# Optimization experiments

Measured on AMD Instinct MI355X. Metric: run time of the kernel, lower is better.

## Reference

```python
import jax, jax.numpy as jnp
import numpy as np

HEADS, OUT_CH = 8, 32  # GATConv(128, 256//8, heads=8) -> concat width 256
NEG_SLOPE = 0.2


def setup_inputs() -> dict:
    key = jax.random.key(0)
    ks = jax.random.split(key, 12)
    N, E, F_IN = 50000, 500000, 128
    H, C = HEADS, OUT_CH
    HID = H * C            # 256
    x = jax.random.normal(ks[0], (N, F_IN), dtype=jnp.float32)
    edge_index = jax.random.randint(ks[1], (2, E), 0, N, dtype=jnp.int64)
    s = 1.0 / np.sqrt(F_IN)
    W_gat = jax.random.normal(ks[2], (F_IN, H * C), dtype=jnp.float32) * s
    att_src = jax.random.normal(ks[3], (H, C), dtype=jnp.float32) * (1.0 / np.sqrt(C))
    att_dst = jax.random.normal(ks[4], (H, C), dtype=jnp.float32) * (1.0 / np.sqrt(C))
    b_gat = jnp.zeros((HID,), dtype=jnp.float32)
    W1 = jax.random.normal(ks[5], (HID, HID // 2), dtype=jnp.float32) * (1.0 / np.sqrt(HID))
    b1 = jnp.zeros((HID // 2,), dtype=jnp.float32)
    W2 = jax.random.normal(ks[6], (HID // 2, 6), dtype=jnp.float32) * (1.0 / np.sqrt(HID // 2))
    b2 = jnp.zeros((6,), dtype=jnp.float32)
    return {"x": x, "edge_index": edge_index, "W_gat": W_gat, "att_src": att_src,
            "att_dst": att_dst, "b_gat": b_gat, "W1": W1, "b1": b1, "W2": W2, "b2": b2}


def _gat_forward(x, edge_index, W_gat, att_src, att_dst, b_gat):
    N = x.shape[0]
    H, C = HEADS, OUT_CH
    # add self loops (PyG GATConv default)
    loop = jnp.arange(N, dtype=edge_index.dtype)
    src = jnp.concatenate([edge_index[0], loop])
    dst = jnp.concatenate([edge_index[1], loop])
    # per-node transform: [N, H, C]
    xh = (x @ W_gat).reshape(N, H, C)
    a_src = jnp.einsum('nhc,hc->nh', xh, att_src)  # [N, H]
    a_dst = jnp.einsum('nhc,hc->nh', xh, att_dst)  # [N, H]
    alpha = a_src[src] + a_dst[dst]                # [Etot, H]
    alpha = jnp.where(alpha >= 0, alpha, NEG_SLOPE * alpha)  # leaky relu
    # segment softmax over destination nodes
    m = jax.ops.segment_max(alpha, dst, num_segments=N)     # [N, H]
    m = jax.lax.stop_gradient(m)
    ex = jnp.exp(alpha - m[dst])
    denom = jax.ops.segment_sum(ex, dst, num_segments=N)    # [N, H]
    coef = ex / denom[dst]                                   # [Etot, H]
    # weighted scatter-add aggregation
    msgs = xh[src] * coef[:, :, None]                        # [Etot, H, C]
    out = jax.ops.segment_sum(msgs, dst, num_segments=N)     # [N, H, C]
    return out.reshape(N, H * C) + b_gat


def reference(x, edge_index, W_gat, att_src, att_dst, b_gat, W1, b1, W2, b2):
    h = _gat_forward(x, edge_index, W_gat, att_src, att_dst, b_gat)
    h = jax.nn.elu(h)
    g = jnp.mean(h, axis=0, keepdims=True)   # [1, 256] mean pool
    g = jax.nn.relu(g @ W1 + b1)
    return g @ W2 + b2                        # [1, 6] logits
```

## Files before the change

### kernel.cpp

```cpp
#include <hip/hip_runtime.h>
#include <hip/hip_fp8.h>
#include <math.h>

#define F_IN 128
#define HID 256
#define NH 8
#define CAP 40
#define BCAP 4096

typedef _Float16 h16;
typedef __attribute__((ext_vector_type(8))) _Float16 half8;
typedef __attribute__((ext_vector_type(4))) float f32x4;

__device__ inline unsigned char f32_to_fp8(float v) {
#if __has_builtin(__builtin_amdgcn_cvt_pk_fp8_f32)
    return (unsigned char)(__builtin_amdgcn_cvt_pk_fp8_f32(v, v, 0, false) & 0xff);
#else
    __hip_fp8_e4m3 t(v);
    return (unsigned char)t.__x;
#endif
}

__device__ inline void fp8x4_to_f32(int w, float* out) {
#if __has_builtin(__builtin_amdgcn_cvt_pk_f32_fp8)
    auto lo = __builtin_amdgcn_cvt_pk_f32_fp8(w, false);
    auto hi = __builtin_amdgcn_cvt_pk_f32_fp8(w, true);
    out[0] = lo[0]; out[1] = lo[1]; out[2] = hi[0]; out[3] = hi[1];
#else
    #pragma unroll
    for (int k = 0; k < 4; ++k) {
        __hip_fp8_e4m3 t;
        t.__x = (unsigned char)((w >> (8 * k)) & 0xff);
        out[k] = (float)t;
    }
#endif
}

__global__ void k_prep(const float* __restrict__ Wg, h16* __restrict__ Wt_sw,
                       int* gcur, float* g2, int n) {
    int i = blockIdx.x * 256 + threadIdx.x;
    if (i < 256) gcur[i] = 0;
    if (i < 256 * HID) g2[i] = 0.f;
    if (i < 4096) {
        int fid = i;
        int lane16 = fid & 15;
        int quad = (fid >> 4) & 3;
        int ks = (fid >> 6) & 3;
        int ct = fid >> 8;
        int col = ct * 16 + lane16;
        int k0 = ks * 32 + quad * 8;
        half8 v;
        #pragma unroll
        for (int j = 0; j < 8; ++j) v[j] = (h16)Wg[(size_t)(k0 + j) * HID + col];
        *(half8*)(Wt_sw + (size_t)fid * 8) = v;
    }
}

__global__ __launch_bounds__(512) void k_ga(const float* __restrict__ x,
                                            const h16* __restrict__ Wt_sw,
                                            const float* __restrict__ att_s,
                                            const float* __restrict__ att_d,
                                            const int* __restrict__ dstp,
                                            const int* __restrict__ srcp,
                                            unsigned char* __restrict__ xh8,
                                            float* __restrict__ a_src,
                                            float* __restrict__ a_dst,
                                            unsigned int* __restrict__ gbuck,
                                            int* __restrict__ gcur,
                                            int n, int e, int ntiles,
                                            int nbuck, int npart) {
    __shared__ __align__(16) char smem[65536];
    int t = threadIdx.x;

    if (blockIdx.x < (unsigned)npart) {
        int* hist  = (int*)smem;
        int* scn   = hist + 256;
        int* lbase = scn + 256;
        int* lcur  = lbase + 256;
        int* base  = lcur + 256;
        unsigned int* sorted = (unsigned int*)(base + 256);
        int c0 = blockIdx.x * 4096;

        if (t < 256) hist[t] = 0;
        __syncthreads();

        unsigned int w8[8];
        int b8[8];
        #pragma unroll
        for (int k = 0; k < 8; ++k) {
            int i = c0 + k * 512 + t;
            if (i < e) {
                int d = dstp[i];
                int s = srcp[i];
                int b = d >> 8;
                b8[k] = b;
                w8[k] = ((unsigned)b << 24) | ((unsigned)(d & 255) << 16) | (unsigned)s;
                atomicAdd(&hist[b], 1);
            } else {
                b8[k] = -1;
                w8[k] = 0;
            }
        }
        __syncthreads();
        if (t < 256) scn[t] = hist[t];
        __syncthreads();
        for (int off = 1; off < 256; off <<= 1) {
            int u = 0;
            if (t < 256 && t >= off) u = scn[t - off];
            __syncthreads();
            if (t < 256 && t >= off) scn[t] += u;
            __syncthreads();
        }
        if (t < 256) {
            lbase[t] = scn[t] - hist[t];
            lcur[t] = 0;
            if (t < nbuck && hist[t] > 0) base[t] = atomicAdd(&gcur[t], hist[t]);
        }
        __syncthreads();
        #pragma unroll
        for (int k = 0; k < 8; ++k) {
            if (b8[k] >= 0) {
                int r = atomicAdd(&lcur[b8[k]], 1);
                sorted[lbase[b8[k]] + r] = w8[k];
            }
        }
        __syncthreads();
        int total = scn[255];
        for (int j = t; j < total; j += 512) {
            unsigned int w = sorted[j];
            int b = w >> 24;
            int addr = base[b] + (j - lbase[b]);
            if (addr < BCAP) gbuck[(size_t)b * BCAP + addr] = w;
        }
        return;
    }

    h16* wlds = (h16*)smem;
    int w = t >> 6, l = t & 63;
    int lane16 = l & 15, quad = l >> 4;

    float4 pv0[4], pv1[4];
    int tile = (blockIdx.x - npart) * 8 + w;
    bool have = tile < ntiles;
    int row0 = tile * 16;
    if (have) {
        int rA = row0 + lane16;
        if (rA >= n) rA = n - 1;
        const float* xrow = x + (size_t)rA * F_IN + quad * 8;
        #pragma unroll
        for (int ks = 0; ks < 4; ++ks) {
            pv0[ks] = *(const float4*)(xrow + ks * 32);
            pv1[ks] = *(const float4*)(xrow + ks * 32 + 4);
        }
    }
    {
        const int4* wsrc = (const int4*)Wt_sw;
        int4* wdst = (int4*)wlds;
        #pragma unroll
        for (int i = 0; i < 8; ++i) wdst[i * 512 + t] = wsrc[i * 512 + t];
    }
    __syncthreads();
    if (!have) return;
    const h16* wl = wlds + (size_t)l * 8;

    half8 afr[4];
    #pragma unroll
    for (int ks = 0; ks < 4; ++ks) {
        half8 a;
        a[0] = (h16)pv0[ks].x; a[1] = (h16)pv0[ks].y;
        a[2] = (h16)pv0[ks].z; a[3] = (h16)pv0[ks].w;
        a[4] = (h16)pv1[ks].x; a[5] = (h16)pv1[ks].y;
        a[6] = (h16)pv1[ks].z; a[7] = (h16)pv1[ks].w;
        afr[ks] = a;
    }
    f32x4 acc[16];
    #pragma unroll
    for (int ct = 0; ct < 16; ++ct) acc[ct] = (f32x4){0.f, 0.f, 0.f, 0.f};
    #pragma unroll
    for (int ct = 0; ct < 16; ++ct) {
        #pragma unroll
        for (int ks = 0; ks < 4; ++ks) {
            half8 bfr = *(const half8*)(wl + (ct * 4 + ks) * 512);
            acc[ct] = __builtin_amdgcn_mfma_f32_16x16x32_f16(afr[ks], bfr, acc[ct], 0, 0, 0);
        }
    }
    if (row0 + 16 <= n) {
        #pragma unroll
        for (int ct = 0; ct < 16; ++ct) {
            int col = ct * 16 + lane16;
            #pragma unroll
            for (int r = 0; r < 4; ++r)
                xh8[(size_t)(row0 + quad * 4 + r) * HID + col] = f32_to_fp8(acc[ct][r]);
        }
    } else {
        #pragma unroll
        for (int ct = 0; ct < 16; ++ct) {
            int col = ct * 16 + lane16;
            #pragma unroll
            for (int r = 0; r < 4; ++r) {
                int row = row0 + quad * 4 + r;
                if (row < n) xh8[(size_t)row * HID + col] = f32_to_fp8(acc[ct][r]);
            }
        }
    }
    #pragma unroll
    for (int h = 0; h < 8; ++h) {
        float ps[4] = {0.f, 0.f, 0.f, 0.f};
        float pd[4] = {0.f, 0.f, 0.f, 0.f};
        #pragma unroll
        for (int cc = 0; cc < 2; ++cc) {
            int ct = h * 2 + cc;
            float as_ = att_s[ct * 16 + lane16];
            float ad_ = att_d[ct * 16 + lane16];
            #pragma unroll
            for (int r = 0; r < 4; ++r) {
                ps[r] += acc[ct][r] * as_;
                pd[r] += acc[ct][r] * ad_;
            }
        }
        #pragma unroll
        for (int m = 1; m < 16; m <<= 1) {
            #pragma unroll
            for (int r = 0; r < 4; ++r) {
                ps[r] += __shfl_xor(ps[r], m, 64);
                pd[r] += __shfl_xor(pd[r], m, 64);
            }
        }
        if (lane16 == 0) {
            #pragma unroll
            for (int r = 0; r < 4; ++r) {
                int row = row0 + quad * 4 + r;
                if (row < n) {
                    a_src[row * NH + h] = ps[r];
                    a_dst[row * NH + h] = pd[r];
                }
            }
        }
    }
}

__global__ __launch_bounds__(256) void k_bin(const unsigned int* __restrict__ gbuck,
                                             const int* __restrict__ gcur,
                                             int* __restrict__ cnt,
                                             unsigned short* __restrict__ bin,
                                             int n, int nbuck) {
    __shared__ int hist[256];
    __shared__ int cur[256];
    __shared__ __align__(16) unsigned short bl[256 * CAP];
    int t = threadIdx.x;
    int b = blockIdx.x;
    int count = gcur[b];
    if (count > BCAP) count = BCAP;
    hist[t] = 0;
    __syncthreads();
    const unsigned int* bb = gbuck + (size_t)b * BCAP;
    for (int j = t; j < count; j += 256) atomicAdd(&hist[(bb[j] >> 16) & 255], 1);
    __syncthreads();
    int node = b * 256 + t;
    if (node < n) {
        int hh = hist[t];
        cnt[node] = hh > CAP ? CAP : hh;
    }
    cur[t] = 0;
    __syncthreads();
    for (int j = t; j < count; j += 256) {
        unsigned int wv = bb[j];
        int dl = (wv >> 16) & 255;
        int pos = atomicAdd(&cur[dl], 1);
        if (pos < CAP) bl[dl * CAP + pos] = (unsigned short)(wv & 0xffff);
    }
    __syncthreads();
    const int4* s4 = (const int4*)bl;
    int4* d4 = (int4*)(bin + (size_t)b * 256 * CAP);
    #pragma unroll
    for (int q = 0; q < 5; ++q) d4[q * 256 + t] = s4[q * 256 + t];
}

__global__ __launch_bounds__(256) void k_agg(const unsigned char* __restrict__ xh8,
                                             const float* __restrict__ a_src,
                                             const float* __restrict__ a_dst,
                                             const int* __restrict__ cnt,
                                             const unsigned short* __restrict__ bin,
                                             const float* __restrict__ b_gat,
                                             float* __restrict__ g2, int n) {
    __shared__ float wpart[4][260];
    int t = threadIdx.x;
    int slot = t >> 4;
    int cl = t & 15;
    int c0 = cl * 16;
    int h = cl >> 1;
    int nn = blockIdx.x * 16 + slot;
    bool alive = nn < n;
    int nnc = alive ? nn : (n - 1);

    float ad = a_dst[nnc * NH + h];
    int deg = cnt[nnc];
    if (deg > CAP) deg = CAP;

    float al = a_src[nnc * NH + h] + ad;
    al = al > 0.f ? al : 0.2f * al;
    float ex = __expf(al);
    float den = ex;
    float acc[16];
    {
        int4 v = *(const int4*)(xh8 + (size_t)nnc * HID + c0);
        float f[16];
        fp8x4_to_f32(v.x, f); fp8x4_to_f32(v.y, f + 4);
        fp8x4_to_f32(v.z, f + 8); fp8x4_to_f32(v.w, f + 12);
        #pragma unroll
        for (int i = 0; i < 16; ++i) acc[i] = ex * f[i];
    }
    const unsigned short* brow = bin + (size_t)nnc * CAP;
    int j = 0;
    for (; j + 4 <= deg; j += 4) {
        ushort4 ss = *(const ushort4*)(brow + j);
        int s0 = ss.x, s1 = ss.y, s2 = ss.z, s3 = ss.w;
        float aa[4];
        aa[0] = a_src[s0 * NH + h];
        aa[1] = a_src[s1 * NH + h];
        aa[2] = a_src[s2 * NH + h];
        aa[3] = a_src[s3 * NH + h];
        int4 v0 = *(const int4*)(xh8 + (size_t)s0 * HID + c0);
        int4 v1 = *(const int4*)(xh8 + (size_t)s1 * HID + c0);
        int4 v2 = *(const int4*)(xh8 + (size_t)s2 * HID + c0);
        int4 v3 = *(const int4*)(xh8 + (size_t)s3 * HID + c0);
        float e4[4];
        #pragma unroll
        for (int q = 0; q < 4; ++q) {
            float a2 = aa[q] + ad;
            a2 = a2 > 0.f ? a2 : 0.2f * a2;
            e4[q] = __expf(a2);
            den += e4[q];
        }
        float f[16];
        fp8x4_to_f32(v0.x, f); fp8x4_to_f32(v0.y, f + 4);
        fp8x4_to_f32(v0.z, f + 8); fp8x4_to_f32(v0.w, f + 12);
        #pragma unroll
        for (int i = 0; i < 16; ++i) acc[i] += e4[0] * f[i];
        fp8x4_to_f32(v1.x, f); fp8x4_to_f32(v1.y, f + 4);
        fp8x4_to_f32(v1.z, f + 8); fp8x4_to_f32(v1.w, f + 12);
        #pragma unroll
        for (int i = 0; i < 16; ++i) acc[i] += e4[1] * f[i];
        fp8x4_to_f32(v2.x, f); fp8x4_to_f32(v2.y, f + 4);
        fp8x4_to_f32(v2.z, f + 8); fp8x4_to_f32(v2.w, f + 12);
        #pragma unroll
        for (int i = 0; i < 16; ++i) acc[i] += e4[2] * f[i];
        fp8x4_to_f32(v3.x, f); fp8x4_to_f32(v3.y, f + 4);
        fp8x4_to_f32(v3.z, f + 8); fp8x4_to_f32(v3.w, f + 12);
        #pragma unroll
        for (int i = 0; i < 16; ++i) acc[i] += e4[3] * f[i];
    }
    for (; j < deg; ++j) {
        int s = brow[j];
        float a2 = a_src[s * NH + h] + ad;
        a2 = a2 > 0.f ? a2 : 0.2f * a2;
        float e2 = __expf(a2);
        den += e2;
        int4 v = *(const int4*)(xh8 + (size_t)s * HID + c0);
        float f[16];
        fp8x4_to_f32(v.x, f); fp8x4_to_f32(v.y, f + 4);
        fp8x4_to_f32(v.z, f + 8); fp8x4_to_f32(v.w, f + 12);
        #pragma unroll
        for (int i = 0; i < 16; ++i) acc[i] += e2 * f[i];
    }
    float inv = 1.f / den;
    float val[16];
    #pragma unroll
    for (int q = 0; q < 4; ++q) {
        float4 bv = *(const float4*)(b_gat + c0 + q * 4);
        val[q * 4 + 0] = acc[q * 4 + 0] * inv + bv.x;
        val[q * 4 + 1] = acc[q * 4 + 1] * inv + bv.y;
        val[q * 4 + 2] = acc[q * 4 + 2] * inv + bv.z;
        val[q * 4 + 3] = acc[q * 4 + 3] * inv + bv.w;
    }
    #pragma unroll
    for (int i = 0; i < 16; ++i) {
        float v = val[i];
        v = v > 0.f ? v : expm1f(v);
        val[i] = alive ? v : 0.f;
    }
    #pragma unroll
    for (int i = 0; i < 16; ++i) {
        val[i] += __shfl_xor(val[i], 16, 64);
        val[i] += __shfl_xor(val[i], 32, 64);
    }
    int w = t >> 6, lw = t & 63;
    if (lw < 16) {
        #pragma unroll
        for (int q = 0; q < 4; ++q)
            *(f32x4*)(&wpart[w][c0 + q * 4]) =
                (f32x4){val[q * 4], val[q * 4 + 1], val[q * 4 + 2], val[q * 4 + 3]};
    }
    __syncthreads();
    float s = wpart[0][t] + wpart[1][t] + wpart[2][t] + wpart[3][t];
    atomicAdd(&g2[(blockIdx.x & 255) * HID + t], s);
}

__global__ __launch_bounds__(256) void k_mlp(const float* __restrict__ g2,
                                             const float* __restrict__ W1,
                                             const float* __restrict__ b1,
                                             const float* __restrict__ W2,
                                             const float* __restrict__ b2,
                                             float* __restrict__ out, int n) {
    __shared__ float gm[HID];
    __shared__ float h1p[2][128];
    __shared__ float h1[128];
    int t = threadIdx.x;
    float s = 0.f;
    for (int b = 0; b < 256; ++b) s += g2[b * HID + t];
    gm[t] = s / (float)n;
    __syncthreads();
    int o = t & 127, hf = t >> 7;
    float a = 0.f;
    #pragma unroll 4
    for (int k = hf * 128; k < hf * 128 + 128; ++k) a += gm[k] * W1[k * 128 + o];
    h1p[hf][o] = a;
    __syncthreads();
    if (t < 128) {
        float v = h1p[0][t] + h1p[1][t] + b1[t];
        h1[t] = v > 0.f ? v : 0.f;
    }
    __syncthreads();
    if (t < 6) {
        float a2 = b2[t];
        for (int k = 0; k < 128; ++k) a2 += h1[k] * W2[k * 6 + t];
        out[t] = a2;
    }
}

extern "C" void kernel_launch(void* const* d_in, const int* in_sizes, int n_in,
                              void* d_out, int out_size, void* d_ws, size_t ws_size,
                              hipStream_t stream) {
    const float* x     = (const float*)d_in[0];
    const int*   ei    = (const int*)d_in[1];
    const float* Wg    = (const float*)d_in[2];
    const float* att_s = (const float*)d_in[3];
    const float* att_d = (const float*)d_in[4];
    const float* b_gat = (const float*)d_in[5];
    const float* W1    = (const float*)d_in[6];
    const float* b1    = (const float*)d_in[7];
    const float* W2    = (const float*)d_in[8];
    const float* b2    = (const float*)d_in[9];

    int N = in_sizes[0] / F_IN;
    int E = in_sizes[1] / 2;
    const int* srcp = ei;
    const int* dstp = ei + E;
    int nblk = (N + 15) / 16;
    int ntiles = (N + 15) / 16;
    int nbuck = (N + 255) >> 8;

    char* ws = (char*)d_ws;
    size_t off = 0;
    auto alloc = [&](size_t bytes) {
        size_t o = off;
        off += (bytes + 255) & ~(size_t)255;
        return o;
    };
    unsigned char* xh8 = (unsigned char*)(ws + alloc((size_t)N * HID));
    h16*   Wt      = (h16*)(ws + alloc((size_t)F_IN * HID * 2));
    float* asr     = (float*)(ws + alloc((size_t)N * NH * 4));
    float* ads     = (float*)(ws + alloc((size_t)N * NH * 4));
    int*   cnt     = (int*)(ws + alloc((size_t)N * 4));
    unsigned short* bin = (unsigned short*)(ws + alloc((size_t)nbuck * 256 * CAP * 2));
    float* g2      = (float*)(ws + alloc((size_t)256 * HID * 4));
    unsigned int* gbuck = (unsigned int*)(ws + alloc((size_t)nbuck * BCAP * 4));
    int*   gcur    = (int*)(ws + alloc((size_t)256 * 4));

    int npart = (E + 4095) / 4096;
    int ngemm = (ntiles + 7) / 8;

    k_prep<<<256, 256, 0, stream>>>(Wg, Wt, gcur, g2, N);
    k_ga<<<npart + ngemm, 512, 0, stream>>>(x, Wt, att_s, att_d, dstp, srcp,
                                            xh8, asr, ads, gbuck, gcur,
                                            N, E, ntiles, nbuck, npart);
    k_bin<<<nbuck, 256, 0, stream>>>(gbuck, gcur, cnt, bin, N, nbuck);
    k_agg<<<nblk, 256, 0, stream>>>(xh8, asr, ads, cnt, bin, b_gat, g2, N);
    k_mlp<<<1, 256, 0, stream>>>(g2, W1, b1, W2, b2, (float*)d_out, N);
}
```

Before: 175.2 us.

## Fold attention vectors into GEMM and make aggregation kernel persistent

Precomputes W_gat·att_src and W_gat·att_dst as an extra 16-column MFMA tile in k_prep, so the attention logits come from one additional MFMA per tile instead of per-head FMAs and shuffle reductions. Separately, k_agg becomes a grid-stride persistent kernel capped at 768 blocks, which accumulates ELU outputs in registers across tiles and so issues fewer atomicAdds into g2. The folded logits are computed from fp16-rounded products, which slightly changes numerics, and k_prep does a serial 32-term dot product per element for the extra tile.

```diff
diff --git a/kernel.cpp b/kernel.cpp
--- a/kernel.cpp
+++ b/kernel.cpp
@@ -7,6 +7,7 @@
 #define NH 8
 #define CAP 40
 #define BCAP 4096
+#define AGG_BLOCKS 768
 
 typedef _Float16 h16;
 typedef __attribute__((ext_vector_type(8))) _Float16 half8;
@@ -36,30 +37,43 @@
 #endif
 }
 
-__global__ void k_prep(const float* __restrict__ Wg, h16* __restrict__ Wt_sw,
+__global__ void k_prep(const float* __restrict__ Wg,
+                       const float* __restrict__ att_s,
+                       const float* __restrict__ att_d,
+                       h16* __restrict__ Wt_sw,
                        int* gcur, float* g2, int n) {
     int i = blockIdx.x * 256 + threadIdx.x;
     if (i < 256) gcur[i] = 0;
     if (i < 256 * HID) g2[i] = 0.f;
-    if (i < 4096) {
+    if (i < 4352) {
         int fid = i;
         int lane16 = fid & 15;
         int quad = (fid >> 4) & 3;
         int ks = (fid >> 6) & 3;
         int ct = fid >> 8;
-        int col = ct * 16 + lane16;
         int k0 = ks * 32 + quad * 8;
         half8 v;
-        #pragma unroll
-        for (int j = 0; j < 8; ++j) v[j] = (h16)Wg[(size_t)(k0 + j) * HID + col];
+        if (ct < 16) {
+            int col = ct * 16 + lane16;
+            #pragma unroll
+            for (int j = 0; j < 8; ++j) v[j] = (h16)Wg[(size_t)(k0 + j) * HID + col];
+        } else {
+            const float* att = (lane16 < 8) ? att_s : att_d;
+            int h = lane16 & 7;
+            #pragma unroll
+            for (int j = 0; j < 8; ++j) {
+                float s = 0.f;
+                for (int c = 0; c < 32; ++c)
+                    s += Wg[(size_t)(k0 + j) * HID + h * 32 + c] * att[h * 32 + c];
+                v[j] = (h16)s;
+            }
+        }
         *(half8*)(Wt_sw + (size_t)fid * 8) = v;
     }
 }
 
 __global__ __launch_bounds__(512) void k_ga(const float* __restrict__ x,
                                             const h16* __restrict__ Wt_sw,
-                                            const float* __restrict__ att_s,
-                                            const float* __restrict__ att_d,
                                             const int* __restrict__ dstp,
                                             const int* __restrict__ srcp,
                                             unsigned char* __restrict__ xh8,
@@ -140,9 +154,15 @@
     int lane16 = l & 15, quad = l >> 4;
 
     float4 pv0[4], pv1[4];
+    half8 bA[4];
     int tile = (blockIdx.x - npart) * 8 + w;
     bool have = tile < ntiles;
     int row0 = tile * 16;
+    {
+        const half8* wq = (const half8*)Wt_sw;
+        #pragma unroll
+        for (int ks = 0; ks < 4; ++ks) bA[ks] = wq[(64 + ks) * 64 + l];
+    }
     if (have) {
         int rA = row0 + lane16;
         if (rA >= n) rA = n - 1;
@@ -184,6 +204,11 @@
             acc[ct] = __builtin_amdgcn_mfma_f32_16x16x32_f16(afr[ks], bfr, acc[ct], 0, 0, 0);
         }
     }
+    f32x4 acc16 = (f32x4){0.f, 0.f, 0.f, 0.f};
+    #pragma unroll
+    for (int ks = 0; ks < 4; ++ks)
+        acc16 = __builtin_amdgcn_mfma_f32_16x16x32_f16(afr[ks], bA[ks], acc16, 0, 0, 0);
+
     if (row0 + 16 <= n) {
         #pragma unroll
         for (int ct = 0; ct < 16; ++ct) {
@@ -192,6 +217,11 @@
             for (int r = 0; r < 4; ++r)
                 xh8[(size_t)(row0 + quad * 4 + r) * HID + col] = f32_to_fp8(acc[ct][r]);
         }
+        float* ap = (lane16 < 8) ? a_src : a_dst;
+        int h = lane16 & 7;
+        #pragma unroll
+        for (int r = 0; r < 4; ++r)
+            ap[(row0 + quad * 4 + r) * NH + h] = acc16[r];
     } else {
         #pragma unroll
         for (int ct = 0; ct < 16; ++ct) {
@@ -202,39 +232,12 @@
                 if (row < n) xh8[(size_t)row * HID + col] = f32_to_fp8(acc[ct][r]);
             }
         }
-    }
-    #pragma unroll
-    for (int h = 0; h < 8; ++h) {
-        float ps[4] = {0.f, 0.f, 0.f, 0.f};
-        float pd[4] = {0.f, 0.f, 0.f, 0.f};
-        #pragma unroll
-        for (int cc = 0; cc < 2; ++cc) {
-            int ct = h * 2 + cc;
-            float as_ = att_s[ct * 16 + lane16];
-            float ad_ = att_d[ct * 16 + lane16];
-            #pragma unroll
-            for (int r = 0; r < 4; ++r) {
-                ps[r] += acc[ct][r] * as_;
-                pd[r] += acc[ct][r] * ad_;
-            }
-        }
-        #pragma unroll
-        for (int m = 1; m < 16; m <<= 1) {
-            #pragma unroll
-            for (int r = 0; r < 4; ++r) {
-                ps[r] += __shfl_xor(ps[r], m, 64);
-                pd[r] += __shfl_xor(pd[r], m, 64);
-            }
-        }
-        if (lane16 == 0) {
-            #pragma unroll
-            for (int r = 0; r < 4; ++r) {
-                int row = row0 + quad * 4 + r;
-                if (row < n) {
-                    a_src[row * NH + h] = ps[r];
-                    a_dst[row * NH + h] = pd[r];
-                }
-            }
+        float* ap = (lane16 < 8) ? a_src : a_dst;
+        int h = lane16 & 7;
+        #pragma unroll
+        for (int r = 0; r < 4; ++r) {
+            int row = row0 + quad * 4 + r;
+            if (row < n) ap[row * NH + h] = acc16[r];
         }
     }
 }
@@ -282,114 +285,124 @@
                                              const int* __restrict__ cnt,
                                              const unsigned short* __restrict__ bin,
                                              const float* __restrict__ b_gat,
-                                             float* __restrict__ g2, int n) {
+                                             float* __restrict__ g2, int n, int ntl) {
     __shared__ float wpart[4][260];
     int t = threadIdx.x;
     int slot = t >> 4;
     int cl = t & 15;
     int c0 = cl * 16;
     int h = cl >> 1;
-    int nn = blockIdx.x * 16 + slot;
-    bool alive = nn < n;
-    int nnc = alive ? nn : (n - 1);
-
-    float ad = a_dst[nnc * NH + h];
-    int deg = cnt[nnc];
-    if (deg > CAP) deg = CAP;
-
-    float al = a_src[nnc * NH + h] + ad;
-    al = al > 0.f ? al : 0.2f * al;
-    float ex = __expf(al);
-    float den = ex;
-    float acc[16];
-    {
-        int4 v = *(const int4*)(xh8 + (size_t)nnc * HID + c0);
-        float f[16];
-        fp8x4_to_f32(v.x, f); fp8x4_to_f32(v.y, f + 4);
-        fp8x4_to_f32(v.z, f + 8); fp8x4_to_f32(v.w, f + 12);
-        #pragma unroll
-        for (int i = 0; i < 16; ++i) acc[i] = ex * f[i];
-    }
-    const unsigned short* brow = bin + (size_t)nnc * CAP;
-    int j = 0;
-    for (; j + 4 <= deg; j += 4) {
-        ushort4 ss = *(const ushort4*)(brow + j);
-        int s0 = ss.x, s1 = ss.y, s2 = ss.z, s3 = ss.w;
-        float aa[4];
-        aa[0] = a_src[s0 * NH + h];
-        aa[1] = a_src[s1 * NH + h];
-        aa[2] = a_src[s2 * NH + h];
-        aa[3] = a_src[s3 * NH + h];
-        int4 v0 = *(const int4*)(xh8 + (size_t)s0 * HID + c0);
-        int4 v1 = *(const int4*)(xh8 + (size_t)s1 * HID + c0);
-        int4 v2 = *(const int4*)(xh8 + (size_t)s2 * HID + c0);
-        int4 v3 = *(const int4*)(xh8 + (size_t)s3 * HID + c0);
-        float e4[4];
+
+    float vacc[16];
+    #pragma unroll
+    for (int i = 0; i < 16; ++i) vacc[i] = 0.f;
+
+    for (int tile = blockIdx.x; tile < ntl; tile += gridDim.x) {
+        int nn = tile * 16 + slot;
+        bool alive = nn < n;
+        int nnc = alive ? nn : (n - 1);
+
+        float ad = a_dst[nnc * NH + h];
+        int deg = cnt[nnc];
+        if (deg > CAP) deg = CAP;
+
+        float al = a_src[nnc * NH + h] + ad;
+        al = al > 0.f ? al : 0.2f * al;
+        float ex = __expf(al);
+        float den = ex;
+        float acc[16];
+        {
+            int4 v = *(const int4*)(xh8 + (size_t)nnc * HID + c0);
+            float f[16];
+            fp8x4_to_f32(v.x, f); fp8x4_to_f32(v.y, f + 4);
+            fp8x4_to_f32(v.z, f + 8); fp8x4_to_f32(v.w, f + 12);
+            #pragma unroll
+            for (int i = 0; i < 16; ++i) acc[i] = ex * f[i];
+        }
+        const unsigned short* brow = bin + (size_t)nnc * CAP;
+        int j = 0;
+        for (; j + 4 <= deg; j += 4) {
+            ushort4 ss = *(const ushort4*)(brow + j);
+            int s0 = ss.x, s1 = ss.y, s2 = ss.z, s3 = ss.w;
+            float aa[4];
+            aa[0] = a_src[s0 * NH + h];
+            aa[1] = a_src[s1 * NH + h];
+            aa[2] = a_src[s2 * NH + h];
+            aa[3] = a_src[s3 * NH + h];
+            int4 v0 = *(const int4*)(xh8 + (size_t)s0 * HID + c0);
+            int4 v1 = *(const int4*)(xh8 + (size_t)s1 * HID + c0);
+            int4 v2 = *(const int4*)(xh8 + (size_t)s2 * HID + c0);
+            int4 v3 = *(const int4*)(xh8 + (size_t)s3 * HID + c0);
+            float e4[4];
+            #pragma unroll
+            for (int q = 0; q < 4; ++q) {
+                float a2 = aa[q] + ad;
+                a2 = a2 > 0.f ? a2 : 0.2f * a2;
+                e4[q] = __expf(a2);
+                den += e4[q];
+            }
+            float f[16];
+            fp8x4_to_f32(v0.x, f); fp8x4_to_f32(v0.y, f + 4);
+            fp8x4_to_f32(v0.z, f + 8); fp8x4_to_f32(v0.w, f + 12);
+            #pragma unroll
+            for (int i = 0; i < 16; ++i) acc[i] += e4[0] * f[i];
+            fp8x4_to_f32(v1.x, f); fp8x4_to_f32(v1.y, f + 4);
+            fp8x4_to_f32(v1.z, f + 8); fp8x4_to_f32(v1.w, f + 12);
+            #pragma unroll
+            for (int i = 0; i < 16; ++i) acc[i] += e4[1] * f[i];
+            fp8x4_to_f32(v2.x, f); fp8x4_to_f32(v2.y, f + 4);
+            fp8x4_to_f32(v2.z, f + 8); fp8x4_to_f32(v2.w, f + 12);
+            #pragma unroll
+            for (int i = 0; i < 16; ++i) acc[i] += e4[2] * f[i];
+            fp8x4_to_f32(v3.x, f); fp8x4_to_f32(v3.y, f + 4);
+            fp8x4_to_f32(v3.z, f + 8); fp8x4_to_f32(v3.w, f + 12);
+            #pragma unroll
+            for (int i = 0; i < 16; ++i) acc[i] += e4[3] * f[i];
+        }
+        for (; j < deg; ++j) {
+            int s = brow[j];
+            float a2 = a_src[s * NH + h] + ad;
+            a2 = a2 > 0.f ? a2 : 0.2f * a2;
+            float e2 = __expf(a2);
+            den += e2;
+            int4 v = *(const int4*)(xh8 + (size_t)s * HID + c0);
+            float f[16];
+            fp8x4_to_f32(v.x, f); fp8x4_to_f32(v.y, f + 4);
+            fp8x4_to_f32(v.z, f + 8); fp8x4_to_f32(v.w, f + 12);
+            #pragma unroll
+            for (int i = 0; i < 16; ++i) acc[i] += e2 * f[i];
+        }
+        float inv = 1.f / den;
         #pragma unroll
         for (int q = 0; q < 4; ++q) {
-            float a2 = aa[q] + ad;
-            a2 = a2 > 0.f ? a2 : 0.2f * a2;
-            e4[q] = __expf(a2);
-            den += e4[q];
-        }
-        float f[16];
-        fp8x4_to_f32(v0.x, f); fp8x4_to_f32(v0.y, f + 4);
-        fp8x4_to_f32(v0.z, f + 8); fp8x4_to_f32(v0.w, f + 12);
-        #pragma unroll
-        for (int i = 0; i < 16; ++i) acc[i] += e4[0] * f[i];
-        fp8x4_to_f32(v1.x, f); fp8x4_to_f32(v1.y, f + 4);
-        fp8x4_to_f32(v1.z, f + 8); fp8x4_to_f32(v1.w, f + 12);
-        #pragma unroll
-        for (int i = 0; i < 16; ++i) acc[i] += e4[1] * f[i];
-        fp8x4_to_f32(v2.x, f); fp8x4_to_f32(v2.y, f + 4);
-        fp8x4_to_f32(v2.z, f + 8); fp8x4_to_f32(v2.w, f + 12);
-        #pragma unroll
-        for (int i = 0; i < 16; ++i) acc[i] += e4[2] * f[i];
-        fp8x4_to_f32(v3.x, f); fp8x4_to_f32(v3.y, f + 4);
-        fp8x4_to_f32(v3.z, f + 8); fp8x4_to_f32(v3.w, f + 12);
-        #pragma unroll
-        for (int i = 0; i < 16; ++i) acc[i] += e4[3] * f[i];
-    }
-    for (; j < deg; ++j) {
-        int s = brow[j];
-        float a2 = a_src[s * NH + h] + ad;
-        a2 = a2 > 0.f ? a2 : 0.2f * a2;
-        float e2 = __expf(a2);
-        den += e2;
-        int4 v = *(const int4*)(xh8 + (size_t)s * HID + c0);
-        float f[16];
-        fp8x4_to_f32(v.x, f); fp8x4_to_f32(v.y, f + 4);
-        fp8x4_to_f32(v.z, f + 8); fp8x4_to_f32(v.w, f + 12);
-        #pragma unroll
-        for (int i = 0; i < 16; ++i) acc[i] += e2 * f[i];
-    }
-    float inv = 1.f / den;
-    float val[16];
-    #pragma unroll
-    for (int q = 0; q < 4; ++q) {
-        float4 bv = *(const float4*)(b_gat + c0 + q * 4);
-        val[q * 4 + 0] = acc[q * 4 + 0] * inv + bv.x;
-        val[q * 4 + 1] = acc[q * 4 + 1] * inv + bv.y;
-        val[q * 4 + 2] = acc[q * 4 + 2] * inv + bv.z;
-        val[q * 4 + 3] = acc[q * 4 + 3] * inv + bv.w;
+            float4 bv = *(const float4*)(b_gat + c0 + q * 4);
+            float v0 = acc[q * 4 + 0] * inv + bv.x;
+            float v1 = acc[q * 4 + 1] * inv + bv.y;
+            float v2 = acc[q * 4 + 2] * inv + bv.z;
+            float v3 = acc[q * 4 + 3] * inv + bv.w;
+            v0 = v0 > 0.f ? v0 : expm1f(v0);
+            v1 = v1 > 0.f ? v1 : expm1f(v1);
+            v2 = v2 > 0.f ? v2 : expm1f(v2);
+            v3 = v3 > 0.f ? v3 : expm1f(v3);
+            if (alive) {
+                vacc[q * 4 + 0] += v0;
+                vacc[q * 4 + 1] += v1;
+                vacc[q * 4 + 2] += v2;
+                vacc[q * 4 + 3] += v3;
+            }
+        }
     }
     #pragma unroll
     for (int i = 0; i < 16; ++i) {
-        float v = val[i];
-        v = v > 0.f ? v : expm1f(v);
-        val[i] = alive ? v : 0.f;
-    }
-    #pragma unroll
-    for (int i = 0; i < 16; ++i) {
-        val[i] += __shfl_xor(val[i], 16, 64);
-        val[i] += __shfl_xor(val[i], 32, 64);
+        vacc[i] += __shfl_xor(vacc[i], 16, 64);
+        vacc[i] += __shfl_xor(vacc[i], 32, 64);
     }
     int w = t >> 6, lw = t & 63;
     if (lw < 16) {
         #pragma unroll
         for (int q = 0; q < 4; ++q)
             *(f32x4*)(&wpart[w][c0 + q * 4]) =
-                (f32x4){val[q * 4], val[q * 4 + 1], val[q * 4 + 2], val[q * 4 + 3]};
+                (f32x4){vacc[q * 4], vacc[q * 4 + 1], vacc[q * 4 + 2], vacc[q * 4 + 3]};
     }
     __syncthreads();
     float s = wpart[0][t] + wpart[1][t] + wpart[2][t] + wpart[3][t];
@@ -458,7 +471,7 @@
         return o;
     };
     unsigned char* xh8 = (unsigned char*)(ws + alloc((size_t)N * HID));
-    h16*   Wt      = (h16*)(ws + alloc((size_t)F_IN * HID * 2));
+    h16*   Wt      = (h16*)(ws + alloc((size_t)4352 * 16));
     float* asr     = (float*)(ws + alloc((size_t)N * NH * 4));
     float* ads     = (float*)(ws + alloc((size_t)N * NH * 4));
     int*   cnt     = (int*)(ws + alloc((size_t)N * 4));
@@ -469,12 +482,13 @@
 
     int npart = (E + 4095) / 4096;
     int ngemm = (ntiles + 7) / 8;
-
-    k_prep<<<256, 256, 0, stream>>>(Wg, Wt, gcur, g2, N);
-    k_ga<<<npart + ngemm, 512, 0, stream>>>(x, Wt, att_s, att_d, dstp, srcp,
+    int naggb = nblk < AGG_BLOCKS ? nblk : AGG_BLOCKS;
+
+    k_prep<<<256, 256, 0, stream>>>(Wg, att_s, att_d, Wt, gcur, g2, N);
+    k_ga<<<npart + ngemm, 512, 0, stream>>>(x, Wt, dstp, srcp,
                                             xh8, asr, ads, gbuck, gcur,
                                             N, E, ntiles, nbuck, npart);
     k_bin<<<nbuck, 256, 0, stream>>>(gbuck, gcur, cnt, bin, N, nbuck);
-    k_agg<<<nblk, 256, 0, stream>>>(xh8, asr, ads, cnt, bin, b_gat, g2, N);
+    k_agg<<<naggb, 256, 0, stream>>>(xh8, asr, ads, cnt, bin, b_gat, g2, N, nblk);
     k_mlp<<<1, 256, 0, stream>>>(g2, W1, b1, W2, b2, (float*)d_out, N);
 }
```

New measurement: 181.7 us. 3.7% more time.
